# Kernel tuning notes

Measured on AMD Instinct MI355X. Metric: run time of the kernel, lower is better.

## Reference

```python
import jax, jax.numpy as jnp
import numpy as np

B, T, N, IN_DIM, H = 8, 16, 1024, 2, 128
HEADS, HD = 8, 16            # HEADS*HD == H (DGL GATConv head-concat)
SNP, SEQ_OUT, DEG = 4, 12, 8
NT = SNP * N                 # nodes per HSTG graph
CKPNT = [4, 7, 10, 13, 16]   # _generate_checkpoints(4, 16)
LRELU = 0.2


def _build_edges():
    # HSTG: per-snapshot spatial edges (random deg-8 adjacency + self-loops)
    # plus identity temporal edges t -> t+1 (uni-direction, non-dense, sync).
    rng = np.random.default_rng(0)
    src, dst = [], []
    ar = np.arange(N)
    for t in range(SNP):
        off = t * N
        src.append(rng.integers(0, N, size=N * DEG) + off)
        dst.append(np.repeat(ar, DEG) + off)
        src.append(ar + off)   # self-loops (keep every dst non-empty)
        dst.append(ar + off)
    for t in range(SNP - 1):
        src.append(ar + t * N)
        dst.append(ar + (t + 1) * N)
    return (jnp.asarray(np.concatenate(src), dtype=jnp.int32),
            jnp.asarray(np.concatenate(dst), dtype=jnp.int32))


def setup_inputs() -> dict:
    key = jax.random.key(0)
    ks = jax.random.split(key, 16)
    edge_src, edge_dst = _build_edges()
    rn = lambda k, s, sc: jax.random.normal(k, s, dtype=jnp.float32) * sc
    return {
        'inputs': rn(ks[0], (B, T, N, IN_DIM), 1.0),
        'W_in': rn(ks[1], (IN_DIM, H), 0.5),
        'b_in': jnp.zeros((H,), jnp.float32),
        'spatial_emb': rn(ks[2], (N, H), 0.05),
        'temporal_emb': rn(ks[3], (N, T), 0.05),
        'gat_w0': rn(ks[4], (H, HEADS * HD), 0.1),
        'gat_al0': rn(ks[5], (HEADS, HD), 0.1),
        'gat_ar0': rn(ks[6], (HEADS, HD), 0.1),
        'gat_b0': jnp.zeros((HEADS * HD,), jnp.float32),
        'gat_w1': rn(ks[7], (H, HEADS * HD), 0.1),
        'gat_al1': rn(ks[8], (HEADS, HD), 0.1),
        'gat_ar1': rn(ks[9], (HEADS, HD), 0.1),
        'gat_b1': jnp.zeros((HEADS * HD,), jnp.float32),
        'agg_q': rn(ks[10], (N, H), 0.1),
        'w_out1': rn(ks[11], (1, SEQ_OUT), 0.5),
        'b_out1': jnp.zeros((SEQ_OUT,), jnp.float32),
        'w_out2': rn(ks[12], (H, 1), 0.1),
        'b_out2': jnp.zeros((1,), jnp.float32),
        'edge_src': edge_src,
        'edge_dst': edge_dst,
    }


def _gat_layer(x, W, a_l, a_r, b, src, dst, activate):
    # x: [NT, H] node features of one graph
    feat = (x @ W).reshape(NT, HEADS, HD)
    el = jnp.sum(feat * a_l, axis=-1)                 # [NT, HEADS]
    er = jnp.sum(feat * a_r, axis=-1)
    e = jax.nn.leaky_relu(el[src] + er[dst], LRELU)    # [E, HEADS]
    m = jax.ops.segment_max(e, dst, num_segments=NT)
    w = jnp.exp(e - m[dst])
    s = jax.ops.segment_sum(w, dst, num_segments=NT)
    alpha = w / s[dst]
    out = jax.ops.segment_sum(feat[src] * alpha[..., None], dst, num_segments=NT)
    out = out.reshape(NT, HEADS * HD) + b
    return jax.nn.elu(out) if activate else out


def reference(inputs, W_in, b_in, spatial_emb, temporal_emb,
              gat_w0, gat_al0, gat_ar0, gat_b0,
              gat_w1, gat_al1, gat_ar1, gat_b1,
              agg_q, w_out1, b_out1, w_out2, b_out2,
              edge_src, edge_dst):
    # input projection + spatial/temporal embeddings
    x = inputs @ W_in + b_in                           # [B,T,N,H]
    x = x + spatial_emb                                # broadcast [N,H]
    x = x + temporal_emb.T[None, :, :, None]           # add temb[n,t] at [b,t,n,h]

    def gat(xb):  # xb: [NT,H], one sample of the batched block-diagonal graph
        h = _gat_layer(xb, gat_w0, gat_al0, gat_ar0, gat_b0, edge_src, edge_dst, True)
        return _gat_layer(h, gat_w1, gat_al1, gat_ar1, gat_b1, edge_src, edge_dst, False)
    gat_b = jax.vmap(gat)

    last = None
    left = 0
    for idx, right in enumerate(CKPNT):
        fs = x[:, left:right]                          # [B, snp or snp-1, N, H]
        if idx != 0:
            fs = jnp.concatenate([last, fs], axis=1)   # [B, SNP, N, H]
        residual = fs
        h = gat_b(fs.reshape(B, NT, H)).reshape(B, SNP, N, H)
        h = h + residual
        # Aggregator: per-node attention over the SNP snapshots -> [B,1,N,H]
        scores = jnp.einsum('btnh,nh->btn', h, agg_q)
        alpha = jax.nn.softmax(scores, axis=1)
        last = jnp.einsum('btn,btnh->bnh', alpha, h)[:, None]
        # LayerNorm over normalized_shape [1,N,H], no affine
        mu = jnp.mean(last, axis=(1, 2, 3), keepdims=True)
        var = jnp.var(last, axis=(1, 2, 3), keepdims=True)
        last = (last - mu) * jax.lax.rsqrt(var + 1e-5)
        left = right

    # decoder (meta_decode = False)
    t = jnp.transpose(last, (0, 3, 2, 1))              # [B,H,N,1]
    o = jax.nn.relu(t @ w_out1 + b_out1)               # [B,H,N,SEQ_OUT]
    o = jnp.transpose(o, (0, 3, 2, 1))                 # [B,SEQ_OUT,N,H]
    return o @ w_out2 + b_out2                         # [B,SEQ_OUT,N,1]
```

## Files before the change

kernel.cpp:

```cpp
#include <hip/hip_runtime.h>
#include <hip/hip_bf16.h>
#include <math.h>

constexpr int kB = 8;
constexpr int kT = 16;
constexpr int kN = 1024;
constexpr int kH = 128;
constexpr int kSNP = 4;
constexpr int kNT = kSNP * kN;
constexpr int kRows = kB * kNT;
constexpr int kSeqOut = 12;
constexpr float kLRelu = 0.2f;
constexpr int kEdgePerSnap = kN * 8 + kN;
constexpr int kSelfOff = kN * 8;
constexpr int kTempBase = kSNP * kEdgePerSnap;
constexpr int kStatsPerIter = kB * 8 * 16;

__global__ void build_fs(const float* __restrict__ inputs, const float* __restrict__ W_in,
                         const float* __restrict__ b_in, const float* __restrict__ spatial,
                         const float* __restrict__ temporal, const float* __restrict__ last,
                         const float* __restrict__ stats, float* __restrict__ A,
                         int left, int first) {
  int blk = blockIdx.x;
  int b = blk & 7;
  int inner = blk >> 3;
  int idx4 = (b << 17) | (inner << 8) | threadIdx.x;
  int h4 = idx4 & 31;
  int n  = (idx4 >> 5) & 1023;
  int t  = (idx4 >> 15) & 3;
  float4 out;
  if (!first && t == 0) {
    float s1 = 0.f, s2 = 0.f;
    #pragma unroll
    for (int s = 0; s < 8; ++s) {
      s1 += stats[b * 128 + s * 16];
      s2 += stats[b * 128 + s * 16 + 1];
    }
    const float inv = 1.0f / (float)(kN * kH);
    float mu = s1 * inv;
    float var = s2 * inv - mu * mu;
    float sc = rsqrtf(var + 1e-5f);
    float4 v = *(const float4*)(last + ((size_t)(b * kN + n)) * kH + h4 * 4);
    out.x = (v.x - mu) * sc; out.y = (v.y - mu) * sc;
    out.z = (v.z - mu) * sc; out.w = (v.w - mu) * sc;
  } else {
    int tg = left + t - (first ? 0 : 1);
    float2 iv = *(const float2*)(inputs + ((size_t)((b * kT + tg) * kN + n)) * 2);
    float tv = temporal[n * kT + tg];
    float4 w0 = *(const float4*)(W_in + h4 * 4);
    float4 w1 = *(const float4*)(W_in + kH + h4 * 4);
    float4 bb = *(const float4*)(b_in + h4 * 4);
    float4 sp = *(const float4*)(spatial + n * kH + h4 * 4);
    out.x = iv.x * w0.x + iv.y * w1.x + bb.x + sp.x + tv;
    out.y = iv.x * w0.y + iv.y * w1.y + bb.y + sp.y + tv;
    out.z = iv.x * w0.z + iv.y * w1.z + bb.z + sp.z + tv;
    out.w = iv.x * w0.w + iv.y * w1.w + bb.w + sp.w + tv;
  }
  *(float4*)(A + (size_t)idx4 * 4) = out;
}

__launch_bounds__(256)
__global__ void gemm128(const float* __restrict__ In, const float* __restrict__ W,
                        float* __restrict__ Out) {
  __shared__ float As[32][65];
  __shared__ float Ws[32][128];
  int tid = threadIdx.x;
  int tx = tid & 15, ty = tid >> 4;
  int blk = blockIdx.x;
  int rowblk = ((blk & 7) << 6) | (blk >> 3);
  const float* Ablk = In + (size_t)rowblk * 64 * kH;
  float acc[4][8];
  #pragma unroll
  for (int i = 0; i < 4; ++i)
    #pragma unroll
    for (int j = 0; j < 8; ++j) acc[i][j] = 0.f;

  for (int kt = 0; kt < kH; kt += 32) {
    #pragma unroll
    for (int l = 0; l < 2; ++l) {
      int f = l * 256 + tid;
      int r = f >> 3, c = f & 7;
      float4 v = *(const float4*)(Ablk + (size_t)r * kH + kt + c * 4);
      int k0 = c * 4;
      As[k0 + 0][r] = v.x; As[k0 + 1][r] = v.y;
      As[k0 + 2][r] = v.z; As[k0 + 3][r] = v.w;
    }
    #pragma unroll
    for (int l = 0; l < 4; ++l) {
      int f = l * 256 + tid;
      int kr = f >> 5, c = f & 31;
      *(float4*)&Ws[kr][c * 4] = *(const float4*)(W + (size_t)(kt + kr) * kH + c * 4);
    }
    __syncthreads();
    #pragma unroll
    for (int kk = 0; kk < 32; ++kk) {
      float4 av = *(const float4*)&As[kk][ty * 4];
      float4 b0 = *(const float4*)&Ws[kk][tx * 4];
      float4 b1 = *(const float4*)&Ws[kk][64 + tx * 4];
      float a[4] = {av.x, av.y, av.z, av.w};
      float bv[8] = {b0.x, b0.y, b0.z, b0.w, b1.x, b1.y, b1.z, b1.w};
      #pragma unroll
      for (int i = 0; i < 4; ++i)
        #pragma unroll
        for (int j = 0; j < 8; ++j) acc[i][j] += a[i] * bv[j];
    }
    __syncthreads();
  }
  int row0 = rowblk * 64 + ty * 4;
  #pragma unroll
  for (int i = 0; i < 4; ++i) {
    float4 o0 = {acc[i][0], acc[i][1], acc[i][2], acc[i][3]};
    float4 o1 = {acc[i][4], acc[i][5], acc[i][6], acc[i][7]};
    *(float4*)(Out + (size_t)(row0 + i) * kH + tx * 4) = o0;
    *(float4*)(Out + (size_t)(row0 + i) * kH + 64 + tx * 4) = o1;
  }
}

__global__ void elr_kernel(const float* __restrict__ feat, const float* __restrict__ al,
                           const float* __restrict__ ar, float* __restrict__ el,
                           float* __restrict__ er) {
  int blk = blockIdx.x;
  int g = ((blk & 7) << 15) | ((blk >> 3) << 8) | threadIdx.x;
  int h = g & 7;
  int node = g >> 3;
  const float4* f = (const float4*)(feat + (size_t)node * kH + h * 16);
  const float4* L = (const float4*)(al + h * 16);
  const float4* R = (const float4*)(ar + h * 16);
  float sl = 0.f, sr = 0.f;
  #pragma unroll
  for (int j = 0; j < 4; ++j) {
    float4 v = f[j], a = L[j], r = R[j];
    sl += v.x * a.x + v.y * a.y + v.z * a.z + v.w * a.w;
    sr += v.x * r.x + v.y * r.y + v.z * r.z + v.w * r.w;
  }
  el[g] = sl;
  er[g] = sr;
}

template <int LAYER>
__launch_bounds__(256)
__global__ void agg_kernel(const float* __restrict__ feat, const float* __restrict__ el,
                           const float* __restrict__ er, const int* __restrict__ esrc,
                           const float* __restrict__ bias, const float* __restrict__ resid,
                           float* __restrict__ outp) {
  int blk = blockIdx.x;
  int b = blk & 7;
  int inner = blk >> 3;
  int tid = threadIdx.x;
  int v = inner * 16 + (tid >> 4);
  int h2 = tid & 15;
  int h = h2 >> 1;
  int t = v >> 10;
  int n = v & 1023;
  int bv = (b << 12) + v;

  int srcs[10];
  int base8 = t * kEdgePerSnap + n * 8;
  #pragma unroll
  for (int k = 0; k < 8; ++k) srcs[k] = esrc[base8 + k];
  srcs[8] = esrc[t * kEdgePerSnap + kSelfOff + n];
  float erv = er[bv * 8 + h];
  int ebase = b << 15;

  float e[10];
  float m = -1e30f;
  #pragma unroll
  for (int i = 0; i < 9; ++i) {
    float x = el[ebase + srcs[i] * 8 + h] + erv;
    x = x > 0.f ? x : kLRelu * x;
    e[i] = x;
    m = fmaxf(m, x);
  }
  if (t > 0) {
    int s9 = esrc[kTempBase + (t - 1) * kN + n];
    srcs[9] = s9;
    float x = el[ebase + s9 * 8 + h] + erv;
    x = x > 0.f ? x : kLRelu * x;
    e[9] = x;
    m = fmaxf(m, x);
  } else {
    srcs[9] = v;
    e[9] = -1e30f;
  }
  float s = 0.f;
  #pragma unroll
  for (int i = 0; i < 10; ++i) { e[i] = expf(e[i] - m); s += e[i]; }
  float inv = 1.0f / s;

  float4 acc0 = {0,0,0,0}, acc1 = {0,0,0,0};
  size_t fbase = (size_t)(b << 12) * kH;
  #pragma unroll
  for (int i = 0; i < 10; ++i) {
    float w = e[i] * inv;
    const float4* fp = (const float4*)(feat + fbase + (size_t)srcs[i] * kH + h2 * 8);
    float4 v0 = fp[0], v1 = fp[1];
    acc0.x += w * v0.x; acc0.y += w * v0.y; acc0.z += w * v0.z; acc0.w += w * v0.w;
    acc1.x += w * v1.x; acc1.y += w * v1.y; acc1.z += w * v1.z; acc1.w += w * v1.w;
  }
  size_t ob = (size_t)bv * kH + h2 * 8;
  const float4* bb = (const float4*)(bias + h2 * 8);
  float4 accs[2] = {acc0, acc1};
  #pragma unroll
  for (int j = 0; j < 2; ++j) {
    float4 a = accs[j], bj = bb[j];
    float4 o;
    if (LAYER == 0) {
      float x0 = a.x + bj.x, x1 = a.y + bj.y, x2 = a.z + bj.z, x3 = a.w + bj.w;
      o.x = x0 > 0.f ? x0 : expm1f(x0);
      o.y = x1 > 0.f ? x1 : expm1f(x1);
      o.z = x2 > 0.f ? x2 : expm1f(x2);
      o.w = x3 > 0.f ? x3 : expm1f(x3);
    } else {
      float4 r = *(const float4*)(resid + ob + j * 4);
      o.x = a.x + bj.x + r.x; o.y = a.y + bj.y + r.y;
      o.z = a.z + bj.z + r.z; o.w = a.w + bj.w + r.w;
    }
    *(float4*)(outp + ob + j * 4) = o;
  }
}

__global__ void attn_kernel(const float* __restrict__ hbuf, const float* __restrict__ q,
                            float* __restrict__ last, float* __restrict__ stats) {
  __shared__ float sred[8];
  int tid = threadIdx.x;
  int wave = tid >> 6, lane = tid & 63;
  int blk = blockIdx.x;
  int b = blk & 7;
  int inner = blk >> 3;
  int d0 = lane * 2;
  float p1 = 0.f, p2 = 0.f;
  for (int i = 0; i < 4; ++i) {
    int n = inner * 16 + wave * 4 + i;
    float2 qv = *(const float2*)(q + (size_t)n * kH + d0);
    float2 hv[4];
    float sc[4];
    #pragma unroll
    for (int t = 0; t < 4; ++t) {
      hv[t] = *(const float2*)(hbuf + ((size_t)(b * kNT + t * kN + n)) * kH + d0);
      float p = hv[t].x * qv.x + hv[t].y * qv.y;
      #pragma unroll
      for (int s = 1; s < 64; s <<= 1) p += __shfl_xor(p, s, 64);
      sc[t] = p;
    }
    float m = fmaxf(fmaxf(sc[0], sc[1]), fmaxf(sc[2], sc[3]));
    float a0 = expf(sc[0] - m), a1 = expf(sc[1] - m);
    float a2 = expf(sc[2] - m), a3 = expf(sc[3] - m);
    float id = 1.0f / (a0 + a1 + a2 + a3);
    float lx = (a0 * hv[0].x + a1 * hv[1].x + a2 * hv[2].x + a3 * hv[3].x) * id;
    float ly = (a0 * hv[0].y + a1 * hv[1].y + a2 * hv[2].y + a3 * hv[3].y) * id;
    float2 lo = {lx, ly};
    *(float2*)(last + ((size_t)(b * kN + n)) * kH + d0) = lo;
    p1 += lx + ly;
    p2 += lx * lx + ly * ly;
  }
  #pragma unroll
  for (int s = 1; s < 64; s <<= 1) {
    p1 += __shfl_xor(p1, s, 64);
    p2 += __shfl_xor(p2, s, 64);
  }
  if (lane == 0) { sred[wave * 2] = p1; sred[wave * 2 + 1] = p2; }
  __syncthreads();
  if (tid == 0) {
    int slot = inner & 7;
    atomicAdd(&stats[b * 128 + slot * 16],     sred[0] + sred[2] + sred[4] + sred[6]);
    atomicAdd(&stats[b * 128 + slot * 16 + 1], sred[1] + sred[3] + sred[5] + sred[7]);
  }
}

__global__ void out_kernel(const float* __restrict__ last, const float* __restrict__ stats,
                           const float* __restrict__ w1, const float* __restrict__ b1,
                           const float* __restrict__ w2, const float* __restrict__ b2,
                           float* __restrict__ out) {
  int tid = threadIdx.x;
  int wave = tid >> 6, lane = tid & 63;
  int gw = blockIdx.x * 4 + wave;
  int b = gw >> 10, n = gw & 1023;
  float s1 = 0.f, s2 = 0.f;
  #pragma unroll
  for (int s = 0; s < 8; ++s) {
    s1 += stats[b * 128 + s * 16];
    s2 += stats[b * 128 + s * 16 + 1];
  }
  const float inv = 1.0f / (float)(kN * kH);
  float mu = s1 * inv;
  float var = s2 * inv - mu * mu;
  float scv = rsqrtf(var + 1e-5f);
  int d0 = lane * 2;
  float2 lv = *(const float2*)(last + ((size_t)(b * kN + n)) * kH + d0);
  float x0 = (lv.x - mu) * scv, x1 = (lv.y - mu) * scv;
  float w20 = w2[d0], w21 = w2[d0 + 1];
  float bias2 = b2[0];
  #pragma unroll
  for (int s = 0; s < kSeqOut; ++s) {
    float w1s = w1[s], b1s = b1[s];
    float v = fmaxf(x0 * w1s + b1s, 0.f) * w20 + fmaxf(x1 * w1s + b1s, 0.f) * w21;
    #pragma unroll
    for (int k = 1; k < 64; k <<= 1) v += __shfl_xor(v, k, 64);
    if (lane == 0) out[(size_t)(b * kSeqOut + s) * kN + n] = v + bias2;
  }
}

extern "C" void kernel_launch(void* const* d_in, const int* in_sizes, int n_in,
                              void* d_out, int out_size, void* d_ws, size_t ws_size,
                              hipStream_t stream) {
  const float* inputs   = (const float*)d_in[0];
  const float* W_in     = (const float*)d_in[1];
  const float* b_in     = (const float*)d_in[2];
  const float* spatial  = (const float*)d_in[3];
  const float* temporal = (const float*)d_in[4];
  const float* gw0      = (const float*)d_in[5];
  const float* gal0     = (const float*)d_in[6];
  const float* gar0     = (const float*)d_in[7];
  const float* gb0      = (const float*)d_in[8];
  const float* gw1      = (const float*)d_in[9];
  const float* gal1     = (const float*)d_in[10];
  const float* gar1     = (const float*)d_in[11];
  const float* gb1      = (const float*)d_in[12];
  const float* aggq     = (const float*)d_in[13];
  const float* w_out1   = (const float*)d_in[14];
  const float* b_out1   = (const float*)d_in[15];
  const float* w_out2   = (const float*)d_in[16];
  const float* b_out2   = (const float*)d_in[17];
  const int*   esrc     = (const int*)d_in[18];

  float* ws = (float*)d_ws;
  float* A     = ws;
  float* Bf    = ws + 4194304;
  float* C     = ws + 8388608;
  float* el    = ws + 12582912;
  float* er    = ws + 12845056;
  float* last  = ws + 13107200;
  float* stats = ws + 14155776;

  hipMemsetAsync(stats, 0, 5 * kStatsPerIter * sizeof(float), stream);

  const int lefts[5] = {0, 4, 7, 10, 13};
  for (int it = 0; it < 5; ++it) {
    const float* st_prev = (it == 0) ? stats : (stats + (it - 1) * kStatsPerIter);
    build_fs<<<4096, 256, 0, stream>>>(inputs, W_in, b_in, spatial, temporal,
                                       last, st_prev, A, lefts[it], it == 0 ? 1 : 0);
    gemm128<<<kRows / 64, 256, 0, stream>>>(A, gw0, Bf);
    elr_kernel<<<1024, 256, 0, stream>>>(Bf, gal0, gar0, el, er);
    agg_kernel<0><<<2048, 256, 0, stream>>>(Bf, el, er, esrc, gb0, nullptr, C);
    gemm128<<<kRows / 64, 256, 0, stream>>>(C, gw1, Bf);
    elr_kernel<<<1024, 256, 0, stream>>>(Bf, gal1, gar1, el, er);
    agg_kernel<1><<<2048, 256, 0, stream>>>(Bf, el, er, esrc, gb1, A, C);
    attn_kernel<<<512, 256, 0, stream>>>(C, aggq, last, stats + it * kStatsPerIter);
  }
  out_kernel<<<2048, 256, 0, stream>>>(last, stats + 4 * kStatsPerIter, w_out1, b_out1,
                                       w_out2, b_out2, (float*)d_out);
}
```

Before: 566.4 us.

## Replace FP32 GEMM with split-bf16 MFMA GEMM and fuse el/er computation

Replaces the scalar FP32 128x128 projection GEMM with a matrix-core kernel. It splits each fp32 operand into high and low bf16 parts and runs three MFMA passes (hi*hi, lo*hi, hi*lo) to keep near-fp32 accuracy. Weights are held in registers and the A tile is staged in XOR-swizzled LDS. The per-head attention logits el/er are computed in the GEMM epilogue with lane shuffles, which removes the separate elr kernel and its re-read of the features. The costs are 3x the MFMA work, the conversion overhead, and scattered scalar output stores.

```diff
diff --git a/kernel.cpp b/kernel.cpp
--- a/kernel.cpp
+++ b/kernel.cpp
@@ -15,6 +15,9 @@
 constexpr int kSelfOff = kN * 8;
 constexpr int kTempBase = kSNP * kEdgePerSnap;
 constexpr int kStatsPerIter = kB * 8 * 16;
+
+typedef __bf16 bf16x8 __attribute__((ext_vector_type(8)));
+typedef float f32x4 __attribute__((ext_vector_type(4)));
 
 __global__ void build_fs(const float* __restrict__ inputs, const float* __restrict__ W_in,
                          const float* __restrict__ b_in, const float* __restrict__ spatial,
@@ -60,81 +63,125 @@
 }
 
 __launch_bounds__(256)
-__global__ void gemm128(const float* __restrict__ In, const float* __restrict__ W,
-                        float* __restrict__ Out) {
-  __shared__ float As[32][65];
-  __shared__ float Ws[32][128];
+__global__ void gemm_mfma(const float* __restrict__ In, const float* __restrict__ W,
+                          const float* __restrict__ gal, const float* __restrict__ gar,
+                          float* __restrict__ Out, float* __restrict__ elp,
+                          float* __restrict__ erp) {
+  __shared__ unsigned short AhL[64 * 128];
+  __shared__ unsigned short AlL[64 * 128];
   int tid = threadIdx.x;
-  int tx = tid & 15, ty = tid >> 4;
+  int lane = tid & 63, wid = tid >> 6;
   int blk = blockIdx.x;
   int rowblk = ((blk & 7) << 6) | (blk >> 3);
-  const float* Ablk = In + (size_t)rowblk * 64 * kH;
-  float acc[4][8];
-  #pragma unroll
-  for (int i = 0; i < 4; ++i)
-    #pragma unroll
-    for (int j = 0; j < 8; ++j) acc[i][j] = 0.f;
-
-  for (int kt = 0; kt < kH; kt += 32) {
-    #pragma unroll
-    for (int l = 0; l < 2; ++l) {
-      int f = l * 256 + tid;
-      int r = f >> 3, c = f & 7;
-      float4 v = *(const float4*)(Ablk + (size_t)r * kH + kt + c * 4);
-      int k0 = c * 4;
-      As[k0 + 0][r] = v.x; As[k0 + 1][r] = v.y;
-      As[k0 + 2][r] = v.z; As[k0 + 3][r] = v.w;
-    }
-    #pragma unroll
-    for (int l = 0; l < 4; ++l) {
-      int f = l * 256 + tid;
-      int kr = f >> 5, c = f & 31;
-      *(float4*)&Ws[kr][c * 4] = *(const float4*)(W + (size_t)(kt + kr) * kH + c * 4);
-    }
-    __syncthreads();
-    #pragma unroll
-    for (int kk = 0; kk < 32; ++kk) {
-      float4 av = *(const float4*)&As[kk][ty * 4];
-      float4 b0 = *(const float4*)&Ws[kk][tx * 4];
-      float4 b1 = *(const float4*)&Ws[kk][64 + tx * 4];
-      float a[4] = {av.x, av.y, av.z, av.w};
-      float bv[8] = {b0.x, b0.y, b0.z, b0.w, b1.x, b1.y, b1.z, b1.w};
-      #pragma unroll
-      for (int i = 0; i < 4; ++i)
-        #pragma unroll
-        for (int j = 0; j < 8; ++j) acc[i][j] += a[i] * bv[j];
-    }
-    __syncthreads();
-  }
-  int row0 = rowblk * 64 + ty * 4;
-  #pragma unroll
-  for (int i = 0; i < 4; ++i) {
-    float4 o0 = {acc[i][0], acc[i][1], acc[i][2], acc[i][3]};
-    float4 o1 = {acc[i][4], acc[i][5], acc[i][6], acc[i][7]};
-    *(float4*)(Out + (size_t)(row0 + i) * kH + tx * 4) = o0;
-    *(float4*)(Out + (size_t)(row0 + i) * kH + 64 + tx * 4) = o1;
-  }
-}
-
-__global__ void elr_kernel(const float* __restrict__ feat, const float* __restrict__ al,
-                           const float* __restrict__ ar, float* __restrict__ el,
-                           float* __restrict__ er) {
-  int blk = blockIdx.x;
-  int g = ((blk & 7) << 15) | ((blk >> 3) << 8) | threadIdx.x;
-  int h = g & 7;
-  int node = g >> 3;
-  const float4* f = (const float4*)(feat + (size_t)node * kH + h * 16);
-  const float4* L = (const float4*)(al + h * 16);
-  const float4* R = (const float4*)(ar + h * 16);
-  float sl = 0.f, sr = 0.f;
-  #pragma unroll
-  for (int j = 0; j < 4; ++j) {
-    float4 v = f[j], a = L[j], r = R[j];
-    sl += v.x * a.x + v.y * a.y + v.z * a.z + v.w * a.w;
-    sr += v.x * r.x + v.y * r.y + v.z * r.z + v.w * r.w;
-  }
-  el[g] = sl;
-  er[g] = sr;
+  int blockRow0 = rowblk * 64;
+
+  union BU { unsigned short u[8]; bf16x8 v; };
+  BU bh[2][4], bl[2][4];
+  int colL = lane & 15;
+  int kgrp = (lane >> 4) * 8;
+  #pragma unroll
+  for (int c = 0; c < 2; ++c) {
+    int col = wid * 32 + c * 16 + colL;
+    #pragma unroll
+    for (int s = 0; s < 4; ++s) {
+      #pragma unroll
+      for (int j = 0; j < 8; ++j) {
+        int k = s * 32 + kgrp + j;
+        float w = W[k * kH + col];
+        unsigned int bits = __float_as_uint(w);
+        bh[c][s].u[j] = (unsigned short)(bits >> 16);
+        float hif = __uint_as_float(bits & 0xffff0000u);
+        bl[c][s].u[j] = (unsigned short)(__float_as_uint(w - hif) >> 16);
+      }
+    }
+  }
+
+  const float* Ablk = In + (size_t)blockRow0 * kH;
+  #pragma unroll
+  for (int itn = 0; itn < 8; ++itn) {
+    int fid = itn * 256 + tid;
+    int row = fid >> 5, kq = fid & 31;
+    float4 v = *(const float4*)(Ablk + (size_t)row * kH + kq * 4);
+    ushort4 hi, lo;
+    unsigned int bx = __float_as_uint(v.x);
+    hi.x = bx >> 16; lo.x = __float_as_uint(v.x - __uint_as_float(bx & 0xffff0000u)) >> 16;
+    unsigned int by = __float_as_uint(v.y);
+    hi.y = by >> 16; lo.y = __float_as_uint(v.y - __uint_as_float(by & 0xffff0000u)) >> 16;
+    unsigned int bz = __float_as_uint(v.z);
+    hi.z = bz >> 16; lo.z = __float_as_uint(v.z - __uint_as_float(bz & 0xffff0000u)) >> 16;
+    unsigned int bw = __float_as_uint(v.w);
+    hi.w = bw >> 16; lo.w = __float_as_uint(v.w - __uint_as_float(bw & 0xffff0000u)) >> 16;
+    int boff = (row * 256 + kq * 8) ^ ((row & 7) << 4);
+    *(ushort4*)((char*)AhL + boff) = hi;
+    *(ushort4*)((char*)AlL + boff) = lo;
+  }
+  __syncthreads();
+
+  f32x4 acc[4][2];
+  #pragma unroll
+  for (int rb = 0; rb < 4; ++rb)
+    #pragma unroll
+    for (int c = 0; c < 2; ++c) acc[rb][c] = (f32x4){0.f, 0.f, 0.f, 0.f};
+
+  #pragma unroll
+  for (int s = 0; s < 4; ++s) {
+    bf16x8 ah[4], alr[4];
+    #pragma unroll
+    for (int rb = 0; rb < 4; ++rb) {
+      int row = rb * 16 + colL;
+      int boff = (row * 256 + s * 64 + (lane >> 4) * 16) ^ ((row & 7) << 4);
+      ah[rb]  = *(const bf16x8*)((const char*)AhL + boff);
+      alr[rb] = *(const bf16x8*)((const char*)AlL + boff);
+    }
+    #pragma unroll
+    for (int c = 0; c < 2; ++c) {
+      #pragma unroll
+      for (int rb = 0; rb < 4; ++rb)
+        acc[rb][c] = __builtin_amdgcn_mfma_f32_16x16x32_bf16(ah[rb], bh[c][s].v, acc[rb][c], 0, 0, 0);
+      #pragma unroll
+      for (int rb = 0; rb < 4; ++rb)
+        acc[rb][c] = __builtin_amdgcn_mfma_f32_16x16x32_bf16(alr[rb], bh[c][s].v, acc[rb][c], 0, 0, 0);
+      #pragma unroll
+      for (int rb = 0; rb < 4; ++rb)
+        acc[rb][c] = __builtin_amdgcn_mfma_f32_16x16x32_bf16(ah[rb], bl[c][s].v, acc[rb][c], 0, 0, 0);
+    }
+  }
+
+  int rquad = (lane >> 4) * 4;
+  #pragma unroll
+  for (int c = 0; c < 2; ++c) {
+    int h = wid * 2 + c;
+    float alv = gal[h * 16 + colL];
+    float arv = gar[h * 16 + colL];
+    int col = wid * 32 + c * 16 + colL;
+    #pragma unroll
+    for (int rb = 0; rb < 4; ++rb) {
+      f32x4 a = acc[rb][c];
+      int row0g = blockRow0 + rb * 16 + rquad;
+      #pragma unroll
+      for (int r = 0; r < 4; ++r)
+        Out[(size_t)(row0g + r) * kH + col] = a[r];
+      float e0 = a[0] * alv, e1 = a[1] * alv, e2 = a[2] * alv, e3 = a[3] * alv;
+      float f0 = a[0] * arv, f1 = a[1] * arv, f2 = a[2] * arv, f3 = a[3] * arv;
+      #pragma unroll
+      for (int m = 1; m < 16; m <<= 1) {
+        e0 += __shfl_xor(e0, m, 64); e1 += __shfl_xor(e1, m, 64);
+        e2 += __shfl_xor(e2, m, 64); e3 += __shfl_xor(e3, m, 64);
+        f0 += __shfl_xor(f0, m, 64); f1 += __shfl_xor(f1, m, 64);
+        f2 += __shfl_xor(f2, m, 64); f3 += __shfl_xor(f3, m, 64);
+      }
+      if (colL == 0) {
+        elp[(size_t)(row0g + 0) * 8 + h] = e0;
+        elp[(size_t)(row0g + 1) * 8 + h] = e1;
+        elp[(size_t)(row0g + 2) * 8 + h] = e2;
+        elp[(size_t)(row0g + 3) * 8 + h] = e3;
+        erp[(size_t)(row0g + 0) * 8 + h] = f0;
+        erp[(size_t)(row0g + 1) * 8 + h] = f1;
+        erp[(size_t)(row0g + 2) * 8 + h] = f2;
+        erp[(size_t)(row0g + 3) * 8 + h] = f3;
+      }
+    }
+  }
 }
 
 template <int LAYER>
@@ -339,11 +386,9 @@
     const float* st_prev = (it == 0) ? stats : (stats + (it - 1) * kStatsPerIter);
     build_fs<<<4096, 256, 0, stream>>>(inputs, W_in, b_in, spatial, temporal,
                                        last, st_prev, A, lefts[it], it == 0 ? 1 : 0);
-    gemm128<<<kRows / 64, 256, 0, stream>>>(A, gw0, Bf);
-    elr_kernel<<<1024, 256, 0, stream>>>(Bf, gal0, gar0, el, er);
+    gemm_mfma<<<kRows / 64, 256, 0, stream>>>(A, gw0, gal0, gar0, Bf, el, er);
     agg_kernel<0><<<2048, 256, 0, stream>>>(Bf, el, er, esrc, gb0, nullptr, C);
-    gemm128<<<kRows / 64, 256, 0, stream>>>(C, gw1, Bf);
-    elr_kernel<<<1024, 256, 0, stream>>>(Bf, gal1, gar1, el, er);
+    gemm_mfma<<<kRows / 64, 256, 0, stream>>>(C, gw1, gal1, gar1, Bf, el, er);
     agg_kernel<1><<<2048, 256, 0, stream>>>(Bf, el, er, esrc, gb1, A, C);
     attn_kernel<<<512, 256, 0, stream>>>(C, aggq, last, stats + it * kStatsPerIter);
   }
```

Measured after the change: 487.3 us. 1.16x faster.
